# Performance work log

Measured on AMD Instinct MI355X. Metric: run time of the kernel, lower is better.

The kernel has to match this reference:

```python
import jax, jax.numpy as jnp
import numpy as np
import math

B, T, C, H = 4, 1024, 1024, 16
R = 32.0
MAX_SPAN = 1024  # block_size
SPAN_REG = 2e-06


def setup_inputs() -> dict:
    key = jax.random.key(0)
    k1, k2, k3 = jax.random.split(key, 3)
    x = jax.random.normal(k1, (B, T, C), dtype=jnp.float32)
    Wqkv = jax.random.normal(k2, (C, 3 * C), dtype=jnp.float32) * 0.02
    Wproj = jax.random.normal(k3, (C, C), dtype=jnp.float32) * 0.02
    span_params = jnp.zeros((H,), dtype=jnp.float32)
    stride_params = jnp.zeros((H, 2), dtype=jnp.float32)
    return {"x": x, "Wqkv": Wqkv, "Wproj": Wproj,
            "span_params": span_params, "stride_params": stride_params}


def reference(x, Wqkv, Wproj, span_params, stride_params):
    b, t, c = x.shape
    h = span_params.shape[0]
    hd = c // h

    qkv = x @ Wqkv                                  # [B,T,3C]
    q, k, v = jnp.split(qkv, 3, axis=-1)
    q = q.reshape(b, t, h, hd).transpose(0, 2, 1, 3)  # [B,H,T,hd]
    k = k.reshape(b, t, h, hd).transpose(0, 2, 1, 3)
    v = v.reshape(b, t, h, hd).transpose(0, 2, 1, 3)

    att = jnp.einsum('bhqd,bhkd->bhqk', q, k) * (1.0 / math.sqrt(hd))

    i = jnp.arange(t)[:, None]
    j = jnp.arange(t)[None, :]
    rel = (i - j).astype(jnp.float32)               # relative position i-j
    causal = i >= j                                 # stride-1 pattern == tril
    allowed2 = (i == j) | ((i > j) & ((i - j) % 2 == 0))  # stride-2 pattern

    spans = jax.nn.sigmoid(span_params) * MAX_SPAN  # [H]
    sw = jax.nn.softmax(stride_params, axis=-1)     # [H,2]

    sp = spans[:, None, None]                       # [H,1,1]
    # soft ramp mask: 1 inside span, linear falloff over R, 0 outside / disallowed
    m1 = jnp.where(causal,  jnp.clip((R + sp - rel) / R, 0.0, 1.0), 0.0)  # [H,T,T]
    m2 = jnp.where(allowed2, jnp.clip((R + sp - rel) / R, 0.0, 1.0), 0.0)
    mask = sw[:, 0, None, None] * m1 + sw[:, 1, None, None] * m2          # [H,T,T]

    # unnormalized exp weighting (no max-subtraction), causal -inf fill
    wexp = jnp.exp(jnp.where(causal, att, -jnp.inf)) * mask               # [B,H,T,T]
    att_n = wexp / jnp.sum(wexp, axis=-1, keepdims=True)

    y = jnp.einsum('bhqk,bhkd->bhqd', att_n, v)
    y = y.transpose(0, 2, 1, 3).reshape(b, t, c)
    y = y @ Wproj

    span_loss = SPAN_REG * jnp.sum(spans) / h
    return y, span_loss
```

## Files before the change

### kernel.cpp

```cpp
#include <hip/hip_runtime.h>
#include <math.h>

#define BATCH 4
#define SEQ   1024
#define CH    1024
#define NH    16
#define HD    64
#define N3    3072

typedef unsigned short u16;
typedef unsigned int   u32;
typedef __attribute__((ext_vector_type(8))) __bf16 bf16x8;
typedef __attribute__((ext_vector_type(4))) float  f32x4;
typedef __attribute__((ext_vector_type(4))) u32    u32x4;

__device__ __forceinline__ u32 f2bf(float f) {
    u32 x = __float_as_uint(f);
    return (x + 0x7fffu + ((x >> 16) & 1u)) >> 16;
}

__device__ __forceinline__ void gload_lds16(const u16* g, u16* l) {
    __builtin_amdgcn_global_load_lds(
        (const __attribute__((address_space(1))) void*)g,
        (__attribute__((address_space(3))) void*)l, 16, 0, 0);
}

__global__ __launch_bounds__(256) void prep_kernel(
    const float* __restrict__ x, const float* __restrict__ Wqkv,
    const float* __restrict__ Wproj,
    u16* __restrict__ xb, u16* __restrict__ wqT, u16* __restrict__ wpT)
{
    __shared__ float tile[32][33];
    const int blk = blockIdx.x;
    if (blk < 2048) {
        int i = (blk * 256 + threadIdx.x) * 8;
        float4 a = *(const float4*)&x[i];
        float4 b = *(const float4*)&x[i + 4];
        int4 p;
        p.x = (int)(f2bf(a.x) | (f2bf(a.y) << 16));
        p.y = (int)(f2bf(a.z) | (f2bf(a.w) << 16));
        p.z = (int)(f2bf(b.x) | (f2bf(b.y) << 16));
        p.w = (int)(f2bf(b.z) | (f2bf(b.w) << 16));
        *(int4*)&xb[i] = p;
        return;
    }
    const int bx2 = blk - 2048;
    int nt = bx2 & 127;
    const int kt = bx2 >> 7;
    const float* W;
    u16* WT;
    int N;
    if (nt < 96) { W = Wqkv; WT = wqT; N = N3; }
    else         { nt -= 96; W = Wproj; WT = wpT; N = CH; }
    const int n0 = nt * 32, k0 = kt * 32;
    const int tx = threadIdx.x & 31, ty = threadIdx.x >> 5;
    #pragma unroll
    for (int p = 0; p < 4; p++)
        tile[ty + p * 8][tx] = W[(size_t)(k0 + ty + p * 8) * N + n0 + tx];
    __syncthreads();
    #pragma unroll
    for (int p = 0; p < 4; p++)
        WT[(size_t)(n0 + ty + p * 8) * CH + k0 + tx] = (u16)f2bf(tile[tx][ty + p * 8]);
}

__global__ __launch_bounds__(256) void gemm_qkv_mfma(
    const u16* __restrict__ A, const u16* __restrict__ BT,
    u16* __restrict__ qb, u16* __restrict__ kbuf, u16* __restrict__ vtb)
{
    __shared__ __align__(16) u16 As[128 * 32];
    __shared__ __align__(16) u16 Bs[128 * 32];

    const int tid = threadIdx.x;
    const int lane = tid & 63;
    const int w = tid >> 6;
    const int wr = w >> 1, wc = w & 1;
    const int m0 = blockIdx.y * 128, n0 = blockIdx.x * 128;

    const int srow = lane >> 2;
    const int sk   = (lane & 3) * 8;
    const u16* gA0 = A  + (size_t)(m0 + w * 16 + srow) * CH + sk;
    const u16* gA1 = A  + (size_t)(m0 + (w + 4) * 16 + srow) * CH + sk;
    const u16* gB0 = BT + (size_t)(n0 + w * 16 + srow) * CH + sk;
    const u16* gB1 = BT + (size_t)(n0 + (w + 4) * 16 + srow) * CH + sk;
    u16* lA0 = As + w * 16 * 32;
    u16* lA1 = As + (w + 4) * 16 * 32;
    u16* lB0 = Bs + w * 16 * 32;
    u16* lB1 = Bs + (w + 4) * 16 * 32;

    const int ln = lane & 15, quad = lane >> 4;
    const int afo = (wr * 64 + ln) * 32 + quad * 8;
    const int bfo = (wc * 64 + ln) * 32 + quad * 8;

    f32x4 acc[4][4];
    #pragma unroll
    for (int i = 0; i < 4; i++)
        #pragma unroll
        for (int j = 0; j < 4; j++) acc[i][j] = (f32x4)(0.f);

    for (int k0 = 0; k0 < CH; k0 += 32) {
        __syncthreads();
        gload_lds16(gA0 + k0, lA0);
        gload_lds16(gA1 + k0, lA1);
        gload_lds16(gB0 + k0, lB0);
        gload_lds16(gB1 + k0, lB1);
        __syncthreads();
        bf16x8 af[4], bfr[4];
        #pragma unroll
        for (int mi = 0; mi < 4; mi++) af[mi]  = *(const bf16x8*)&As[afo + mi * 512];
        #pragma unroll
        for (int ni = 0; ni < 4; ni++) bfr[ni] = *(const bf16x8*)&Bs[bfo + ni * 512];
        #pragma unroll
        for (int mi = 0; mi < 4; mi++)
            #pragma unroll
            for (int ni = 0; ni < 4; ni++)
                acc[mi][ni] = __builtin_amdgcn_mfma_f32_16x16x32_bf16(
                    af[mi], bfr[ni], acc[mi][ni], 0, 0, 0);
    }

    const int which = (n0 >> 10);
    if (which == 2) {
        #pragma unroll
        for (int ni = 0; ni < 4; ni++) {
            const int n = n0 + wc * 64 + ni * 16 + ln;
            const int h = (n >> 6) & 15;
            const int d = n & 63;
            #pragma unroll
            for (int mi = 0; mi < 4; mi++) {
                const int m = m0 + wr * 64 + mi * 16 + quad * 4;
                const int b = m >> 10, t = m & 1023;
                int2 pv;
                pv.x = (int)(f2bf(acc[mi][ni][0]) | (f2bf(acc[mi][ni][1]) << 16));
                pv.y = (int)(f2bf(acc[mi][ni][2]) | (f2bf(acc[mi][ni][3]) << 16));
                *(int2*)&vtb[(((size_t)(b * NH + h)) * HD + d) * SEQ + t] = pv;
            }
        }
    } else {
        u16* dst = (which == 0) ? qb : kbuf;
        #pragma unroll
        for (int ni = 0; ni < 4; ni++) {
            const int n = n0 + wc * 64 + ni * 16 + ln;
            const int h = (n >> 6) & 15;
            const int d = n & 63;
            #pragma unroll
            for (int mi = 0; mi < 4; mi++) {
                #pragma unroll
                for (int r = 0; r < 4; r++) {
                    const int m = m0 + wr * 64 + mi * 16 + quad * 4 + r;
                    const int b = m >> 10, t = m & 1023;
                    dst[(((size_t)(b * NH + h)) * SEQ + t) * HD + d] =
                        (u16)f2bf(acc[mi][ni][r]);
                }
            }
        }
    }
}

__global__ __launch_bounds__(256) void gemm_proj_mfma(
    const u16* __restrict__ A, const u16* __restrict__ BT, float* __restrict__ out,
    const float* __restrict__ sp, float* __restrict__ loss_out)
{
    __shared__ __align__(16) u16 As[64 * 32];
    __shared__ __align__(16) u16 Bs[128 * 32];

    const int tid = threadIdx.x;
    const int lane = tid & 63;
    const int w = tid >> 6;
    const int wr = w >> 1, wc = w & 1;
    const int m0 = blockIdx.y * 64, n0 = blockIdx.x * 128;

    if (blockIdx.x == 0 && blockIdx.y == 0 && tid == 0) {
        float s = 0.f;
        #pragma unroll
        for (int h = 0; h < NH; h++) {
            float sig = 1.f / (1.f + __expf(-sp[h]));
            s += sig * 1024.f;
        }
        loss_out[0] = 2e-6f * s / (float)NH;
    }

    const int srow = lane >> 2;
    const int sk   = (lane & 3) * 8;
    const u16* gA0 = A  + (size_t)(m0 + w * 16 + srow) * CH + sk;
    const u16* gB0 = BT + (size_t)(n0 + w * 16 + srow) * CH + sk;
    const u16* gB1 = BT + (size_t)(n0 + (w + 4) * 16 + srow) * CH + sk;
    u16* lA0 = As + w * 16 * 32;
    u16* lB0 = Bs + w * 16 * 32;
    u16* lB1 = Bs + (w + 4) * 16 * 32;

    const int ln = lane & 15, quad = lane >> 4;
    const int afo = (wr * 32 + ln) * 32 + quad * 8;
    const int bfo = (wc * 64 + ln) * 32 + quad * 8;

    f32x4 acc[2][4];
    #pragma unroll
    for (int i = 0; i < 2; i++)
        #pragma unroll
        for (int j = 0; j < 4; j++) acc[i][j] = (f32x4)(0.f);

    for (int k0 = 0; k0 < CH; k0 += 32) {
        __syncthreads();
        gload_lds16(gA0 + k0, lA0);
        gload_lds16(gB0 + k0, lB0);
        gload_lds16(gB1 + k0, lB1);
        __syncthreads();
        bf16x8 af[2], bfr[4];
        #pragma unroll
        for (int mi = 0; mi < 2; mi++) af[mi]  = *(const bf16x8*)&As[afo + mi * 512];
        #pragma unroll
        for (int ni = 0; ni < 4; ni++) bfr[ni] = *(const bf16x8*)&Bs[bfo + ni * 512];
        #pragma unroll
        for (int mi = 0; mi < 2; mi++)
            #pragma unroll
            for (int ni = 0; ni < 4; ni++)
                acc[mi][ni] = __builtin_amdgcn_mfma_f32_16x16x32_bf16(
                    af[mi], bfr[ni], acc[mi][ni], 0, 0, 0);
    }

    #pragma unroll
    for (int ni = 0; ni < 4; ni++) {
        const int n = n0 + wc * 64 + ni * 16 + ln;
        #pragma unroll
        for (int mi = 0; mi < 2; mi++) {
            #pragma unroll
            for (int r = 0; r < 4; r++) {
                const int m = m0 + wr * 32 + mi * 16 + quad * 4 + r;
                out[(size_t)m * CH + n] = acc[mi][ni][r];
            }
        }
    }
}

__global__ __launch_bounds__(256) void attn_mfma_kernel(
    const u16* __restrict__ qg, const u16* __restrict__ kg,
    const u16* __restrict__ vt,
    const float* __restrict__ span_params, const float* __restrict__ stride_params,
    u16* __restrict__ yb)
{
    __shared__ __align__(16) u16 Ks[2][64 * 64];
    __shared__ __align__(16) u16 Vs[2][64 * 64];
    __shared__ __align__(16) u16 Ps[4][16 * 64];

    const int tid  = threadIdx.x;
    const int lane = tid & 63;
    const int w    = tid >> 6;
    const int ln   = lane & 15, quad = lane >> 4;
    const int lm7  = ln & 7;

    const int blk = blockIdx.x;
    const int bh  = blk & 63;
    const int it  = 15 - (blk >> 6);
    const int h   = bh & (NH - 1);
    const int b   = bh >> 4;
    const int it0 = it << 6;
    const int row_base = it0 + (w << 4);

    const float span  = 1024.f / (1.f + __expf(-span_params[h]));
    const float limit = 32.f + span;
    const float e0 = __expf(stride_params[2 * h + 0]);
    const float e1 = __expf(stride_params[2 * h + 1]);
    const float swO = e0 / (e0 + e1);
    const float c1 = limit * (1.f / 32.f);

    const size_t hb  = (size_t)bh * SEQ;
    const size_t hvt = (size_t)bh * HD;

    const u16* qp = qg + (hb + row_base + ln) * HD + quad * 8;
    bf16x8 aq0 = *(const bf16x8*)qp;
    bf16x8 aq1 = *(const bf16x8*)(qp + 32);

    u32x4 onesw; onesw.x = onesw.y = onesw.z = onesw.w = 0x3f803f80u;
    const bf16x8 onesf = __builtin_bit_cast(bf16x8, onesw);

    f32x4 acc_o[4];
    #pragma unroll
    for (int di = 0; di < 4; di++) acc_o[di] = (f32x4)(0.f);
    f32x4 acc_s = (f32x4)(0.f);

    int jmin = it0 - (int)limit - 1;
    if (jmin < 0) jmin = 0;
    const int jt0 = jmin & ~63;

    const int srow = lane >> 3;
    const int schk = lane & 7;
    const int cs   = schk ^ srow;
    const int ra   = w * 8 + srow;
    const u16* pk0 = kg + (hb + ra) * HD + cs * 8;
    const u16* pk1 = pk0 + 32 * HD;
    const u16* pv0 = vt + (hvt + ra) * SEQ + cs * 8;
    const u16* pv1 = pv0 + 32 * SEQ;

    u16* Psw = Ps[w];

    gload_lds16(pk0 + (size_t)jt0 * HD, &Ks[0][w * 512]);
    gload_lds16(pk1 + (size_t)jt0 * HD, &Ks[0][2048 + w * 512]);
    gload_lds16(pv0 + jt0,              &Vs[0][w * 512]);
    gload_lds16(pv1 + jt0,              &Vs[0][2048 + w * 512]);

    int cur = 0;
    for (int jt = jt0; jt <= it0; jt += 64, cur ^= 1) {
        __syncthreads();

        const int nxt = jt + 64;
        if (nxt <= it0) {
            gload_lds16(pk0 + (size_t)nxt * HD, &Ks[cur ^ 1][w * 512]);
            gload_lds16(pk1 + (size_t)nxt * HD, &Ks[cur ^ 1][2048 + w * 512]);
            gload_lds16(pv0 + nxt,              &Vs[cur ^ 1][w * 512]);
            gload_lds16(pv1 + nxt,              &Vs[cur ^ 1][2048 + w * 512]);
        }

        const u16* Kc = Ks[cur];
        const u16* Vc = Vs[cur];

        bool sk[4];
        #pragma unroll
        for (int ni = 0; ni < 4; ni++) {
            const int col0 = jt + ni * 16;
            sk[ni] = (row_base + 15 < col0) ||
                     ((float)(row_base - (col0 + 15)) >= limit);
        }
        const bool nz0 = !sk[0] || !sk[1];
        const bool nz1 = !sk[2] || !sk[3];

        #pragma unroll
        for (int ni = 0; ni < 4; ni++) {
            const int col0 = jt + ni * 16;
            const int cbase = ni * 2 + (ln >> 3);
            if (sk[ni]) {
                if ((ni < 2) ? nz0 : nz1) {
                    #pragma unroll
                    for (int r = 0; r < 4; r++) {
                        const int il = quad * 4 + r;
                        Psw[il * 64 + (cbase ^ (il & 7)) * 8 + lm7] = 0;
                    }
                }
                continue;
            }
            const int krow = ni * 16 + ln;
            bf16x8 bk0 = *(const bf16x8*)&Kc[krow * 64 + ((quad ^ lm7) * 8)];
            bf16x8 bk1 = *(const bf16x8*)&Kc[krow * 64 + (((quad + 4) ^ lm7) * 8)];
            f32x4 s = __builtin_amdgcn_mfma_f32_16x16x32_bf16(aq0, bk0, (f32x4)(0.f), 0, 0, 0);
            s = __builtin_amdgcn_mfma_f32_16x16x32_bf16(aq1, bk1, s, 0, 0, 0);
            #pragma unroll
            for (int r = 0; r < 4; r++) {
                const int il  = quad * 4 + r;
                const int rel = (row_base + il) - (col0 + ln);
                float clip = fminf(fmaxf(fmaf((float)rel, -(1.f / 32.f), c1), 0.f), 1.f);
                float fac  = (rel & 1) ? swO : 1.0f;
                float wt   = (rel < 0) ? 0.f : clip * fac;
                float wv   = __expf(s[r] * 0.125f) * wt;
                Psw[il * 64 + (cbase ^ (il & 7)) * 8 + lm7] = (u16)f2bf(wv);
            }
        }

        if (nz0) {
            bf16x8 ap0 = *(const bf16x8*)&Psw[ln * 64 + (quad ^ lm7) * 8];
            acc_s = __builtin_amdgcn_mfma_f32_16x16x32_bf16(ap0, onesf, acc_s, 0, 0, 0);
            #pragma unroll
            for (int di = 0; di < 4; di++) {
                const int vrow = di * 16 + ln;
                bf16x8 bv0 = *(const bf16x8*)&Vc[vrow * 64 + ((quad ^ lm7) * 8)];
                acc_o[di] = __builtin_amdgcn_mfma_f32_16x16x32_bf16(ap0, bv0, acc_o[di], 0, 0, 0);
            }
        }
        if (nz1) {
            bf16x8 ap1 = *(const bf16x8*)&Psw[ln * 64 + ((quad + 4) ^ lm7) * 8];
            acc_s = __builtin_amdgcn_mfma_f32_16x16x32_bf16(ap1, onesf, acc_s, 0, 0, 0);
            #pragma unroll
            for (int di = 0; di < 4; di++) {
                const int vrow = di * 16 + ln;
                bf16x8 bv1 = *(const bf16x8*)&Vc[vrow * 64 + (((quad + 4) ^ lm7) * 8)];
                acc_o[di] = __builtin_amdgcn_mfma_f32_16x16x32_bf16(ap1, bv1, acc_o[di], 0, 0, 0);
            }
        }
    }

    #pragma unroll
    for (int r = 0; r < 4; r++) {
        const int t = row_base + quad * 4 + r;
        const float inv = 1.f / acc_s[r];
        const size_t rowoff = ((size_t)(b * SEQ + t)) * CH + h * HD;
        #pragma unroll
        for (int di = 0; di < 4; di++)
            yb[rowoff + di * 16 + ln] = (u16)f2bf(acc_o[di][r] * inv);
    }
}

extern "C" void kernel_launch(void* const* d_in, const int* in_sizes, int n_in,
                              void* d_out, int out_size, void* d_ws, size_t ws_size,
                              hipStream_t stream)
{
    const float* x            = (const float*)d_in[0];
    const float* Wqkv         = (const float*)d_in[1];
    const float* Wproj        = (const float*)d_in[2];
    const float* span_params  = (const float*)d_in[3];
    const float* stride_param = (const float*)d_in[4];
    float* out = (float*)d_out;

    const size_t SZ = (size_t)BATCH * NH * SEQ * HD;
    u16* base = (u16*)d_ws;
    u16* qb  = base;
    u16* kb  = qb + SZ;
    u16* vtb = kb + SZ;
    u16* yb  = vtb + SZ;
    u16* xb  = yb + SZ;
    u16* wqT = xb + SZ;
    u16* wpT = wqT + (size_t)CH * N3;

    prep_kernel<<<dim3(6144), 256, 0, stream>>>(x, Wqkv, Wproj, xb, wqT, wpT);

    gemm_qkv_mfma<<<dim3(N3 / 128, (BATCH * SEQ) / 128), 256, 0, stream>>>(
        xb, wqT, qb, kb, vtb);

    attn_mfma_kernel<<<dim3(BATCH * NH * (SEQ / 64)), 256, 0, stream>>>(
        qb, kb, vtb, span_params, stride_param, yb);

    gemm_proj_mfma<<<dim3(CH / 128, (BATCH * SEQ) / 64), 256, 0, stream>>>(
        yb, wpT, out, span_params, out + SZ);
}
```

Measured before the change: 161.2 us.

## Double-buffer LDS and enlarge M tile in projection GEMM

The output projection GEMM now uses 128x128 tiles instead of 64x128, with each wave computing a 64x64 sub-tile (4x4 MFMA accumulators). Its LDS staging is double-buffered: the next k-slice's global-to-LDS loads are issued before computing on the current one, leaving one barrier per iteration instead of two. This is meant to overlap memory latency with MFMA work and raise operand reuse. In exchange it halves the grid to 256 blocks and increases register and LDS use. It also relies on the async LDS loads being complete at the barrier.

Result: no change. 162.0 us (+0.5%).

```diff
diff --git a/kernel.cpp b/kernel.cpp
--- a/kernel.cpp
+++ b/kernel.cpp
@@ -159,14 +159,14 @@
     const u16* __restrict__ A, const u16* __restrict__ BT, float* __restrict__ out,
     const float* __restrict__ sp, float* __restrict__ loss_out)
 {
-    __shared__ __align__(16) u16 As[64 * 32];
-    __shared__ __align__(16) u16 Bs[128 * 32];
+    __shared__ __align__(16) u16 As[2][128 * 32];
+    __shared__ __align__(16) u16 Bs[2][128 * 32];
 
     const int tid = threadIdx.x;
     const int lane = tid & 63;
     const int w = tid >> 6;
     const int wr = w >> 1, wc = w & 1;
-    const int m0 = blockIdx.y * 64, n0 = blockIdx.x * 128;
+    const int m0 = blockIdx.y * 128, n0 = blockIdx.x * 128;
 
     if (blockIdx.x == 0 && blockIdx.y == 0 && tid == 0) {
         float s = 0.f;
@@ -181,35 +181,46 @@
     const int srow = lane >> 2;
     const int sk   = (lane & 3) * 8;
     const u16* gA0 = A  + (size_t)(m0 + w * 16 + srow) * CH + sk;
+    const u16* gA1 = A  + (size_t)(m0 + (w + 4) * 16 + srow) * CH + sk;
     const u16* gB0 = BT + (size_t)(n0 + w * 16 + srow) * CH + sk;
     const u16* gB1 = BT + (size_t)(n0 + (w + 4) * 16 + srow) * CH + sk;
-    u16* lA0 = As + w * 16 * 32;
-    u16* lB0 = Bs + w * 16 * 32;
-    u16* lB1 = Bs + (w + 4) * 16 * 32;
+    const int lo0 = w * 16 * 32;
+    const int lo1 = (w + 4) * 16 * 32;
 
     const int ln = lane & 15, quad = lane >> 4;
-    const int afo = (wr * 32 + ln) * 32 + quad * 8;
+    const int afo = (wr * 64 + ln) * 32 + quad * 8;
     const int bfo = (wc * 64 + ln) * 32 + quad * 8;
 
-    f32x4 acc[2][4];
-    #pragma unroll
-    for (int i = 0; i < 2; i++)
+    f32x4 acc[4][4];
+    #pragma unroll
+    for (int i = 0; i < 4; i++)
         #pragma unroll
         for (int j = 0; j < 4; j++) acc[i][j] = (f32x4)(0.f);
 
-    for (int k0 = 0; k0 < CH; k0 += 32) {
+    gload_lds16(gA0, &As[0][lo0]);
+    gload_lds16(gA1, &As[0][lo1]);
+    gload_lds16(gB0, &Bs[0][lo0]);
+    gload_lds16(gB1, &Bs[0][lo1]);
+
+    int cur = 0;
+    for (int k0 = 0; k0 < CH; k0 += 32, cur ^= 1) {
         __syncthreads();
-        gload_lds16(gA0 + k0, lA0);
-        gload_lds16(gB0 + k0, lB0);
-        gload_lds16(gB1 + k0, lB1);
-        __syncthreads();
-        bf16x8 af[2], bfr[4];
-        #pragma unroll
-        for (int mi = 0; mi < 2; mi++) af[mi]  = *(const bf16x8*)&As[afo + mi * 512];
-        #pragma unroll
-        for (int ni = 0; ni < 4; ni++) bfr[ni] = *(const bf16x8*)&Bs[bfo + ni * 512];
-        #pragma unroll
-        for (int mi = 0; mi < 2; mi++)
+
+        const int nxt = k0 + 32;
+        if (nxt < CH) {
+            gload_lds16(gA0 + nxt, &As[cur ^ 1][lo0]);
+            gload_lds16(gA1 + nxt, &As[cur ^ 1][lo1]);
+            gload_lds16(gB0 + nxt, &Bs[cur ^ 1][lo0]);
+            gload_lds16(gB1 + nxt, &Bs[cur ^ 1][lo1]);
+        }
+
+        bf16x8 af[4], bfr[4];
+        #pragma unroll
+        for (int mi = 0; mi < 4; mi++) af[mi]  = *(const bf16x8*)&As[cur][afo + mi * 512];
+        #pragma unroll
+        for (int ni = 0; ni < 4; ni++) bfr[ni] = *(const bf16x8*)&Bs[cur][bfo + ni * 512];
+        #pragma unroll
+        for (int mi = 0; mi < 4; mi++)
             #pragma unroll
             for (int ni = 0; ni < 4; ni++)
                 acc[mi][ni] = __builtin_amdgcn_mfma_f32_16x16x32_bf16(
@@ -220,10 +231,10 @@
     for (int ni = 0; ni < 4; ni++) {
         const int n = n0 + wc * 64 + ni * 16 + ln;
         #pragma unroll
-        for (int mi = 0; mi < 2; mi++) {
+        for (int mi = 0; mi < 4; mi++) {
             #pragma unroll
             for (int r = 0; r < 4; r++) {
-                const int m = m0 + wr * 32 + mi * 16 + quad * 4 + r;
+                const int m = m0 + wr * 64 + mi * 16 + quad * 4 + r;
                 out[(size_t)m * CH + n] = acc[mi][ni][r];
             }
         }
@@ -414,6 +425,6 @@
     attn_mfma_kernel<<<dim3(BATCH * NH * (SEQ / 64)), 256, 0, stream>>>(
         qb, kb, vtb, span_params, stride_param, yb);
 
-    gemm_proj_mfma<<<dim3(CH / 128, (BATCH * SEQ) / 64), 256, 0, stream>>>(
+    gemm_proj_mfma<<<dim3(CH / 128, (BATCH * SEQ) / 128), 256, 0, stream>>>(
         yb, wpT, out, span_params, out + SZ);
 }
```
